# Optimization experiments

Hardware: AMD Instinct MI355X
Metric: run time of the kernel (lower is better)

The kernel has to match this reference:

```python
import jax, jax.numpy as jnp
import numpy as np

B, S, D, H = 4, 2048, 1024, 16
DEPTH = D // H
NEG = 1e10


def setup_inputs() -> dict:
    key = jax.random.key(0)
    ks = jax.random.split(key, 11)
    sc = 0.02
    return {
        "q": jax.random.normal(ks[0], (B, S, D), jnp.float32),
        "v": jax.random.normal(ks[1], (B, S, D), jnp.float32),
        "k": jax.random.normal(ks[2], (B, S, D), jnp.float32),
        "Wq": jax.random.normal(ks[3], (D, D), jnp.float32) * sc,
        "bq": jnp.zeros((D,), jnp.float32),
        "Wk": jax.random.normal(ks[4], (D, D), jnp.float32) * sc,
        "bk": jnp.zeros((D,), jnp.float32),
        "Wv": jax.random.normal(ks[5], (D, D), jnp.float32) * sc,
        "bv": jnp.zeros((D,), jnp.float32),
        "Wo": jax.random.normal(ks[6], (D, D), jnp.float32) * sc,
        "bo": jnp.zeros((D,), jnp.float32),
        "mask": 1,
    }


def _split_heads(x):
    # [B, S, D] -> [B, H, S, depth]
    b, s, _ = x.shape
    return x.reshape(b, s, H, DEPTH).transpose(0, 2, 1, 3)


def reference(q, v, k, Wq, bq, Wk, bk, Wv, bv, Wo, bo, mask):
    qh = _split_heads(q @ Wq + bq)
    kh = _split_heads(k @ Wk + bk)
    vh = _split_heads(v @ Wv + bv)

    scale = 1.0 / jnp.sqrt(jnp.asarray(DEPTH, jnp.float32))
    # [B, H, Sq, Sk]
    logits = jnp.einsum("bhqd,bhkd->bhqk", qh, kh) * scale

    if mask:
        nd, ns = logits.shape[-2], logits.shape[-1]
        i = jnp.arange(nd)[:, None]
        j = jnp.arange(ns)[None, :]
        b = (i >= j - ns + nd).astype(logits.dtype)  # lower triangle from lower-right
        logits = logits * b - NEG * (1.0 - b)

    attn = jax.nn.softmax(logits, axis=-1)
    out = jnp.einsum("bhqk,bhkd->bhqd", attn, vh)  # [B, H, Sq, depth]
    out = out.transpose(0, 2, 1, 3).reshape(q.shape[0], -1, D)  # concat heads
    return out @ Wo + bo
```

## Files before the change

### kernel.cpp

```cpp
#include <hip/hip_runtime.h>
#include <hip/hip_bf16.h>
#include <cstdint>
#include <cstddef>

#define S_LEN 2048
#define D_MODEL 1024
#define N_HEADS 16
#define DEPTH 64
#define BATCH 4

typedef __attribute__((ext_vector_type(4))) float f32x4;
typedef __attribute__((ext_vector_type(8))) short bf16x8;
typedef __attribute__((ext_vector_type(4))) unsigned short us4;
typedef __attribute__((ext_vector_type(8))) unsigned short us8;

__device__ __forceinline__ unsigned short f2bf(float f) {
  unsigned int u = __builtin_bit_cast(unsigned int, f);
  u += 0x7FFFu + ((u >> 16) & 1u);
  return (unsigned short)(u >> 16);
}

__global__ __launch_bounds__(256) void transpose_cast(const float* __restrict__ W,
                                                      unsigned short* __restrict__ Wt,
                                                      int N, float scale) {
  __shared__ float tile[32][33];
  int bx = blockIdx.x * 32;
  int by = blockIdx.y * 32;
  int tx = threadIdx.x, ty = threadIdx.y;
#pragma unroll
  for (int i = 0; i < 4; ++i)
    tile[ty + i * 8][tx] = W[(size_t)(by + ty + i * 8) * N + bx + tx];
  __syncthreads();
#pragma unroll
  for (int i = 0; i < 4; ++i)
    Wt[(size_t)(bx + ty + i * 8) * N + by + tx] = f2bf(tile[tx][ty + i * 8] * scale);
}

__global__ __launch_bounds__(256) void transpose_v(const unsigned short* __restrict__ Vp,
                                                   unsigned short* __restrict__ Vt) {
  __shared__ unsigned short tile[64][72];
  int tid = threadIdx.x;
  int sb = blockIdx.x;
  int bh = blockIdx.y;
  int b = bh >> 4, h = bh & 15;
  int s0 = sb * 64;
#pragma unroll
  for (int rep = 0; rep < 2; ++rep) {
    int idx = rep * 256 + tid;
    int r = idx >> 3, c8 = idx & 7;
    us8 v = *(const us8*)(Vp + (size_t)(b * S_LEN + s0 + r) * D_MODEL + h * DEPTH + c8 * 8);
#pragma unroll
    for (int e = 0; e < 8; ++e) tile[c8 * 8 + e][r] = v[e];
  }
  __syncthreads();
#pragma unroll
  for (int rep = 0; rep < 2; ++rep) {
    int idx = rep * 256 + tid;
    int d = idx >> 3, c8 = idx & 7;
    us8 v = *(const us8*)&tile[d][c8 * 8];
    *(us8*)(Vt + ((size_t)(bh * DEPTH + d)) * S_LEN + s0 + c8 * 8) = v;
  }
}

template <bool A_IS_F32, bool OUT_F32>
__global__ __launch_bounds__(256) void gemm_bt(const void* __restrict__ Aptr,
                                               const unsigned short* __restrict__ Bt,
                                               const float* __restrict__ bias,
                                               float bias_scale,
                                               void* __restrict__ Cptr,
                                               int M, int N, int K) {
  __shared__ unsigned short a_lds[128][72];
  __shared__ unsigned short b_lds[128][72];

  int tid = threadIdx.x;
  int wave = tid >> 6, lane = tid & 63;
  int l15 = lane & 15, lg = lane >> 4;
  int row0 = blockIdx.x * 128;
  int col0 = blockIdx.y * 128;
  int wm = wave >> 1, wn = wave & 1;

  const float* Af = (const float*)Aptr;
  const unsigned short* Ah = (const unsigned short*)Aptr;

  f32x4 acc[4][4] = {};

  for (int k0 = 0; k0 < K; k0 += 64) {
    __syncthreads();
    if constexpr (A_IS_F32) {
      int r = tid >> 4, c4 = tid & 15;
#pragma unroll
      for (int rep = 0; rep < 8; ++rep) {
        f32x4 v = *(const f32x4*)(Af + (size_t)(row0 + rep * 16 + r) * K + k0 + c4 * 4);
        us4 h = {f2bf(v[0]), f2bf(v[1]), f2bf(v[2]), f2bf(v[3])};
        *(us4*)&a_lds[rep * 16 + r][c4 * 4] = h;
      }
    } else {
      int r = tid >> 3, c8 = tid & 7;
#pragma unroll
      for (int rep = 0; rep < 4; ++rep) {
        us8 v = *(const us8*)(Ah + (size_t)(row0 + rep * 32 + r) * K + k0 + c8 * 8);
        *(us8*)&a_lds[rep * 32 + r][c8 * 8] = v;
      }
    }
    {
      int r = tid >> 3, c8 = tid & 7;
#pragma unroll
      for (int rep = 0; rep < 4; ++rep) {
        us8 v = *(const us8*)(Bt + (size_t)(col0 + rep * 32 + r) * K + k0 + c8 * 8);
        *(us8*)&b_lds[rep * 32 + r][c8 * 8] = v;
      }
    }
    __syncthreads();
#pragma unroll
    for (int kk = 0; kk < 2; ++kk) {
      bf16x8 af[4], bfr[4];
#pragma unroll
      for (int i = 0; i < 4; ++i)
        af[i] = *(const bf16x8*)&a_lds[wm * 64 + i * 16 + l15][kk * 32 + lg * 8];
#pragma unroll
      for (int j = 0; j < 4; ++j)
        bfr[j] = *(const bf16x8*)&b_lds[wn * 64 + j * 16 + l15][kk * 32 + lg * 8];
#pragma unroll
      for (int i = 0; i < 4; ++i)
#pragma unroll
        for (int j = 0; j < 4; ++j)
          acc[i][j] = __builtin_amdgcn_mfma_f32_16x16x32_bf16(af[i], bfr[j], acc[i][j], 0, 0, 0);
    }
  }

#pragma unroll
  for (int i = 0; i < 4; ++i) {
#pragma unroll
    for (int j = 0; j < 4; ++j) {
      int col = col0 + wn * 64 + j * 16 + l15;
      float bv = bias[col] * bias_scale;
#pragma unroll
      for (int r = 0; r < 4; ++r) {
        int row = row0 + wm * 64 + i * 16 + lg * 4 + r;
        float v = acc[i][j][r] + bv;
        if constexpr (OUT_F32)
          ((float*)Cptr)[(size_t)row * N + col] = v;
        else
          ((unsigned short*)Cptr)[(size_t)row * N + col] = f2bf(v);
      }
    }
  }
}

__global__ __launch_bounds__(512) void attn_kernel(const unsigned short* __restrict__ Qp,
                                                   const unsigned short* __restrict__ Kp,
                                                   const unsigned short* __restrict__ Vt,
                                                   unsigned short* __restrict__ Op) {
  __shared__ unsigned short k_lds[2][64][76];
  __shared__ unsigned short vt_lds[2][64][76];
  __shared__ unsigned short p_lds[8][16][76];

  int tid = threadIdx.x;
  int w = tid >> 6, lane = tid & 63;
  int l15 = lane & 15, lg = lane >> 4;

  int bid = blockIdx.x;
  int swz = (bid & 7) * 64 + (bid >> 3);
  int pairIdx = swz & 7;
  int bh = swz >> 3;
  int b = bh >> 4, h = bh & 15;

  const unsigned short* Kbase = Kp + (size_t)b * S_LEN * D_MODEL + h * DEPTH;
  const unsigned short* Vbase = Vt + (size_t)bh * DEPTH * S_LEN;

  bool stageV = (tid >= 256);
  int st = tid & 255;
  int r = st >> 2, cb = (st & 3) * 16;
  const unsigned short* srow = stageV ? (Vbase + (size_t)r * S_LEN + cb)
                                      : (Kbase + (size_t)r * D_MODEL + cb);
  const size_t sstep = stageV ? 64 : (size_t)64 * D_MODEL;

  bf16x8 ones;
#pragma unroll
  for (int e = 0; e < 8; ++e) ones[e] = (short)0x3F80;

  for (int half = 0; half < 2; ++half) {
    int t = (half == 0) ? pairIdx : (15 - pairIdx);
    int q0 = t * 128;
    int nkv = 2 * t + 2;
    int q0w = q0 + w * 16;

    const unsigned short* qp =
        Qp + ((size_t)(b * S_LEN + q0 + w * 16 + l15)) * D_MODEL + h * DEPTH;
    bf16x8 qf0 = *(const bf16x8*)(qp + lg * 8);
    bf16x8 qf1 = *(const bf16x8*)(qp + 32 + lg * 8);

    f32x4 acc_l = (f32x4){0.f, 0.f, 0.f, 0.f};
    f32x4 acc_o[4];
#pragma unroll
    for (int d = 0; d < 4; ++d) acc_o[d] = (f32x4){0.f, 0.f, 0.f, 0.f};

    const unsigned short* sptr = srow;
    us8 s0 = *(const us8*)sptr;
    us8 s1 = *(const us8*)(sptr + 8);
    sptr += sstep;
    __syncthreads();
    if (stageV) {
      *(us8*)&vt_lds[0][r][cb] = s0;
      *(us8*)&vt_lds[0][r][cb + 8] = s1;
    } else {
      *(us8*)&k_lds[0][r][cb] = s0;
      *(us8*)&k_lds[0][r][cb + 8] = s1;
    }

    for (int kb = 0; kb < nkv; ++kb) {
      int cur = kb & 1;
      int k0 = kb * 64;
      __syncthreads();
      bool more = (kb + 1) < nkv;
      if (more) {
        s0 = *(const us8*)sptr;
        s1 = *(const us8*)(sptr + 8);
        sptr += sstep;
      }

      bool full_masked = (k0 > q0w + 15);
      if (!full_masked) {
        f32x4 s[4];
#pragma unroll
        for (int nf = 0; nf < 4; ++nf) s[nf] = (f32x4){0.f, 0.f, 0.f, 0.f};
        __builtin_amdgcn_s_setprio(1);
#pragma unroll
        for (int nf = 0; nf < 4; ++nf) {
          bf16x8 kf0 = *(const bf16x8*)&k_lds[cur][nf * 16 + l15][lg * 8];
          bf16x8 kf1 = *(const bf16x8*)&k_lds[cur][nf * 16 + l15][32 + lg * 8];
          s[nf] = __builtin_amdgcn_mfma_f32_16x16x32_bf16(qf0, kf0, s[nf], 0, 0, 0);
          s[nf] = __builtin_amdgcn_mfma_f32_16x16x32_bf16(qf1, kf1, s[nf], 0, 0, 0);
        }
        __builtin_amdgcn_s_setprio(0);

        bool diag = (k0 + 63 > q0w);
        if (diag) {
#pragma unroll
          for (int nf = 0; nf < 4; ++nf)
#pragma unroll
            for (int rr = 0; rr < 4; ++rr) {
              int qrow = q0w + lg * 4 + rr;
              int kcol = k0 + nf * 16 + l15;
              float x = (kcol > qrow) ? -1e10f : s[nf][rr];
              float p = __builtin_amdgcn_exp2f(x);
              p_lds[w][lg * 4 + rr][nf * 16 + l15] =
                  (unsigned short)(__builtin_bit_cast(unsigned int, p) >> 16);
            }
        } else {
#pragma unroll
          for (int nf = 0; nf < 4; ++nf)
#pragma unroll
            for (int rr = 0; rr < 4; ++rr) {
              float p = __builtin_amdgcn_exp2f(s[nf][rr]);
              p_lds[w][lg * 4 + rr][nf * 16 + l15] =
                  (unsigned short)(__builtin_bit_cast(unsigned int, p) >> 16);
            }
        }

        __builtin_amdgcn_s_setprio(1);
#pragma unroll
        for (int kk = 0; kk < 2; ++kk) {
          bf16x8 pf = *(const bf16x8*)&p_lds[w][l15][kk * 32 + lg * 8];
          acc_l = __builtin_amdgcn_mfma_f32_16x16x32_bf16(pf, ones, acc_l, 0, 0, 0);
#pragma unroll
          for (int d = 0; d < 4; ++d) {
            bf16x8 vf = *(const bf16x8*)&vt_lds[cur][d * 16 + l15][kk * 32 + lg * 8];
            acc_o[d] = __builtin_amdgcn_mfma_f32_16x16x32_bf16(pf, vf, acc_o[d], 0, 0, 0);
          }
        }
        __builtin_amdgcn_s_setprio(0);
      }

      if (more) {
        int nb = cur ^ 1;
        if (stageV) {
          *(us8*)&vt_lds[nb][r][cb] = s0;
          *(us8*)&vt_lds[nb][r][cb + 8] = s1;
        } else {
          *(us8*)&k_lds[nb][r][cb] = s0;
          *(us8*)&k_lds[nb][r][cb + 8] = s1;
        }
      }
    }

#pragma unroll
    for (int rr = 0; rr < 4; ++rr) {
      float inv = 1.0f / acc_l[rr];
      int qrow = q0 + w * 16 + lg * 4 + rr;
      unsigned short* op = Op + ((size_t)(b * S_LEN + qrow)) * D_MODEL + h * DEPTH;
#pragma unroll
      for (int d = 0; d < 4; ++d)
        op[d * 16 + l15] = f2bf(acc_o[d][rr] * inv);
    }
  }
}

extern "C" void kernel_launch(void* const* d_in, const int* in_sizes, int n_in,
                              void* d_out, int out_size, void* d_ws, size_t ws_size,
                              hipStream_t stream) {
  const float* q  = (const float*)d_in[0];
  const float* v  = (const float*)d_in[1];
  const float* k  = (const float*)d_in[2];
  const float* Wq = (const float*)d_in[3];
  const float* bq = (const float*)d_in[4];
  const float* Wk = (const float*)d_in[5];
  const float* bk = (const float*)d_in[6];
  const float* Wv = (const float*)d_in[7];
  const float* bv = (const float*)d_in[8];
  const float* Wo = (const float*)d_in[9];
  const float* bo = (const float*)d_in[10];

  char* ws = (char*)d_ws;
  const size_t WSZ = (size_t)D_MODEL * D_MODEL * 2;
  const size_t XSZ = (size_t)BATCH * S_LEN * D_MODEL * 2;
  unsigned short* Wqt = (unsigned short*)(ws);
  unsigned short* Wkt = (unsigned short*)(ws + WSZ);
  unsigned short* Wvt = (unsigned short*)(ws + 2 * WSZ);
  unsigned short* Wot = (unsigned short*)(ws + 3 * WSZ);
  unsigned short* Qp  = (unsigned short*)(ws + 4 * WSZ);
  unsigned short* Kp  = (unsigned short*)(ws + 4 * WSZ + XSZ);
  unsigned short* Vp  = (unsigned short*)(ws + 4 * WSZ + 2 * XSZ);
  unsigned short* Vtp = (unsigned short*)(ws + 4 * WSZ + 3 * XSZ);
  unsigned short* AO  = Vp;

  const float SCL = 0.125f * 1.4426950408889634f;

  dim3 tb(32, 8);
  dim3 tg(D_MODEL / 32, D_MODEL / 32);
  hipLaunchKernelGGL(transpose_cast, tg, tb, 0, stream, Wq, Wqt, D_MODEL, SCL);
  hipLaunchKernelGGL(transpose_cast, tg, tb, 0, stream, Wk, Wkt, D_MODEL, 1.0f);
  hipLaunchKernelGGL(transpose_cast, tg, tb, 0, stream, Wv, Wvt, D_MODEL, 1.0f);
  hipLaunchKernelGGL(transpose_cast, tg, tb, 0, stream, Wo, Wot, D_MODEL, 1.0f);

  const int M = BATCH * S_LEN;
  dim3 gg(M / 128, D_MODEL / 128);
  hipLaunchKernelGGL((gemm_bt<true, false>), gg, dim3(256), 0, stream,
                     (const void*)q, Wqt, bq, SCL, (void*)Qp, M, D_MODEL, D_MODEL);
  hipLaunchKernelGGL((gemm_bt<true, false>), gg, dim3(256), 0, stream,
                     (const void*)k, Wkt, bk, 1.0f, (void*)Kp, M, D_MODEL, D_MODEL);
  hipLaunchKernelGGL((gemm_bt<true, false>), gg, dim3(256), 0, stream,
                     (const void*)v, Wvt, bv, 1.0f, (void*)Vp, M, D_MODEL, D_MODEL);

  hipLaunchKernelGGL(transpose_v, dim3(S_LEN / 64, BATCH * N_HEADS), dim3(256), 0, stream,
                     Vp, Vtp);

  hipLaunchKernelGGL(attn_kernel, dim3(512), dim3(512), 0, stream, Qp, Kp, Vtp, AO);

  hipLaunchKernelGGL((gemm_bt<false, true>), gg, dim3(256), 0, stream,
                     (const void*)AO, Wot, bo, 1.0f, d_out, M, D_MODEL, D_MODEL);
}
```

Measured before the change: 201.7 us.

## Batch QKV GEMMs into one launch with double-buffered async LDS loads

Measured after the change: 185.6 us. -8.0%, faster.

```diff
diff --git a/kernel.cpp b/kernel.cpp
--- a/kernel.cpp
+++ b/kernel.cpp
@@ -9,6 +9,9 @@
 #define DEPTH 64
 #define BATCH 4
 
+#define GLOBAL_AS __attribute__((address_space(1)))
+#define LDS_AS __attribute__((address_space(3)))
+
 typedef __attribute__((ext_vector_type(4))) float f32x4;
 typedef __attribute__((ext_vector_type(8))) short bf16x8;
 typedef __attribute__((ext_vector_type(4))) unsigned short us4;
@@ -18,6 +21,10 @@
   unsigned int u = __builtin_bit_cast(unsigned int, f);
   u += 0x7FFFu + ((u >> 16) & 1u);
   return (unsigned short)(u >> 16);
+}
+
+__device__ __forceinline__ unsigned short f2bf_hw(float f) {
+  return __builtin_bit_cast(unsigned short, __float2bfloat16(f));
 }
 
 __global__ __launch_bounds__(256) void transpose_cast(const float* __restrict__ W,
@@ -62,86 +69,144 @@
   }
 }
 
+struct GemmSlice {
+  const void* A;
+  const unsigned short* Bt;
+  const float* bias;
+  void* C;
+  float bscale;
+};
+struct GemmArgs {
+  GemmSlice s[3];
+};
+
 template <bool A_IS_F32, bool OUT_F32>
-__global__ __launch_bounds__(256) void gemm_bt(const void* __restrict__ Aptr,
-                                               const unsigned short* __restrict__ Bt,
-                                               const float* __restrict__ bias,
-                                               float bias_scale,
-                                               void* __restrict__ Cptr,
-                                               int M, int N, int K) {
-  __shared__ unsigned short a_lds[128][72];
-  __shared__ unsigned short b_lds[128][72];
+__global__ __launch_bounds__(256) void gemm_bt(GemmArgs args, int M, int N, int K) {
+  constexpr int ASTR = A_IS_F32 ? 72 : 64;
+  __shared__ unsigned short a_lds[2][128 * ASTR];
+  __shared__ unsigned short b_lds[2][128 * 64];
+
+  const GemmSlice& g = args.s[blockIdx.y];
+  const float* Af = (const float*)g.A;
+  const unsigned short* Ah = (const unsigned short*)g.A;
+  const unsigned short* Bt = g.Bt;
 
   int tid = threadIdx.x;
   int wave = tid >> 6, lane = tid & 63;
   int l15 = lane & 15, lg = lane >> 4;
-  int row0 = blockIdx.x * 128;
-  int col0 = blockIdx.y * 128;
   int wm = wave >> 1, wn = wave & 1;
 
-  const float* Af = (const float*)Aptr;
-  const unsigned short* Ah = (const unsigned short*)Aptr;
+  int d = blockIdx.x;
+  int wk = (d & 7) * 64 + (d >> 3);
+  int mi = (wk >> 6) * 8 + ((wk & 63) >> 3);
+  int nj = wk & 7;
+  int row0 = mi * 128, col0 = nj * 128;
 
   f32x4 acc[4][4] = {};
-
-  for (int k0 = 0; k0 < K; k0 += 64) {
-    __syncthreads();
-    if constexpr (A_IS_F32) {
-      int r = tid >> 4, c4 = tid & 15;
-#pragma unroll
-      for (int rep = 0; rep < 8; ++rep) {
-        f32x4 v = *(const f32x4*)(Af + (size_t)(row0 + rep * 16 + r) * K + k0 + c4 * 4);
-        us4 h = {f2bf(v[0]), f2bf(v[1]), f2bf(v[2]), f2bf(v[3])};
-        *(us4*)&a_lds[rep * 16 + r][c4 * 4] = h;
-      }
-    } else {
-      int r = tid >> 3, c8 = tid & 7;
-#pragma unroll
-      for (int rep = 0; rep < 4; ++rep) {
-        us8 v = *(const us8*)(Ah + (size_t)(row0 + rep * 32 + r) * K + k0 + c8 * 8);
-        *(us8*)&a_lds[rep * 32 + r][c8 * 8] = v;
-      }
-    }
-    {
-      int r = tid >> 3, c8 = tid & 7;
-#pragma unroll
-      for (int rep = 0; rep < 4; ++rep) {
-        us8 v = *(const us8*)(Bt + (size_t)(col0 + rep * 32 + r) * K + k0 + c8 * 8);
-        *(us8*)&b_lds[rep * 32 + r][c8 * 8] = v;
-      }
-    }
-    __syncthreads();
+  f32x4 av[8];
+
+  int ar = tid >> 4, ac4 = tid & 15;
+
+  auto loadA = [&](int k0) {
+#pragma unroll
+    for (int rep = 0; rep < 8; ++rep)
+      av[rep] = *(const f32x4*)(Af + (size_t)(row0 + rep * 16 + ar) * K + k0 + ac4 * 4);
+  };
+  auto writeA = [&](int buf) {
+#pragma unroll
+    for (int rep = 0; rep < 8; ++rep) {
+      us4 h = {f2bf_hw(av[rep][0]), f2bf_hw(av[rep][1]),
+               f2bf_hw(av[rep][2]), f2bf_hw(av[rep][3])};
+      *(us4*)&a_lds[buf][(rep * 16 + ar) * 72 + ac4 * 4] = h;
+    }
+  };
+  auto issueA = [&](int buf, int k0) {
+#pragma unroll
+    for (int rep = 0; rep < 4; ++rep) {
+      int chunk = (wave * 4 + rep) * 64 + lane;
+      int row = chunk >> 3;
+      int c8 = (chunk & 7) ^ (row & 7);
+      __builtin_amdgcn_global_load_lds(
+          (const GLOBAL_AS void*)(Ah + (size_t)(row0 + row) * K + k0 + c8 * 8),
+          (LDS_AS void*)(&a_lds[buf][chunk * 8]), 16, 0, 0);
+    }
+  };
+  auto issueB = [&](int buf, int k0) {
+#pragma unroll
+    for (int rep = 0; rep < 4; ++rep) {
+      int chunk = (wave * 4 + rep) * 64 + lane;
+      int row = chunk >> 3;
+      int c8 = (chunk & 7) ^ (row & 7);
+      __builtin_amdgcn_global_load_lds(
+          (const GLOBAL_AS void*)(Bt + (size_t)(col0 + row) * K + k0 + c8 * 8),
+          (LDS_AS void*)(&b_lds[buf][chunk * 8]), 16, 0, 0);
+    }
+  };
+  auto compute = [&](int buf) {
 #pragma unroll
     for (int kk = 0; kk < 2; ++kk) {
       bf16x8 af[4], bfr[4];
 #pragma unroll
-      for (int i = 0; i < 4; ++i)
-        af[i] = *(const bf16x8*)&a_lds[wm * 64 + i * 16 + l15][kk * 32 + lg * 8];
-#pragma unroll
-      for (int j = 0; j < 4; ++j)
-        bfr[j] = *(const bf16x8*)&b_lds[wn * 64 + j * 16 + l15][kk * 32 + lg * 8];
-#pragma unroll
-      for (int i = 0; i < 4; ++i)
-#pragma unroll
-        for (int j = 0; j < 4; ++j)
-          acc[i][j] = __builtin_amdgcn_mfma_f32_16x16x32_bf16(af[i], bfr[j], acc[i][j], 0, 0, 0);
-    }
-  }
-
-#pragma unroll
-  for (int i = 0; i < 4; ++i) {
-#pragma unroll
-    for (int j = 0; j < 4; ++j) {
-      int col = col0 + wn * 64 + j * 16 + l15;
-      float bv = bias[col] * bias_scale;
+      for (int ii = 0; ii < 4; ++ii) {
+        int row = wm * 64 + ii * 16 + l15;
+        if constexpr (A_IS_F32)
+          af[ii] = *(const bf16x8*)&a_lds[buf][row * 72 + kk * 32 + lg * 8];
+        else
+          af[ii] = *(const bf16x8*)&a_lds[buf][row * 64 + ((kk * 4 + lg) ^ (l15 & 7)) * 8];
+      }
+#pragma unroll
+      for (int jj = 0; jj < 4; ++jj) {
+        int row = wn * 64 + jj * 16 + l15;
+        bfr[jj] = *(const bf16x8*)&b_lds[buf][row * 64 + ((kk * 4 + lg) ^ (l15 & 7)) * 8];
+      }
+#pragma unroll
+      for (int ii = 0; ii < 4; ++ii)
+#pragma unroll
+        for (int jj = 0; jj < 4; ++jj)
+          acc[ii][jj] = __builtin_amdgcn_mfma_f32_16x16x32_bf16(af[ii], bfr[jj], acc[ii][jj], 0, 0, 0);
+    }
+  };
+
+  int nk = K >> 6;
+  issueB(0, 0);
+  if constexpr (A_IS_F32) {
+    loadA(0);
+    writeA(0);
+  } else {
+    issueA(0, 0);
+  }
+
+  for (int ki = 0; ki < nk; ++ki) {
+    int cur = ki & 1;
+    __syncthreads();
+    bool more = (ki + 1) < nk;
+    if (more) {
+      issueB(cur ^ 1, (ki + 1) * 64);
+      if constexpr (A_IS_F32)
+        loadA((ki + 1) * 64);
+      else
+        issueA(cur ^ 1, (ki + 1) * 64);
+    }
+    compute(cur);
+    if (more) {
+      if constexpr (A_IS_F32) writeA(cur ^ 1);
+    }
+  }
+
+#pragma unroll
+  for (int ii = 0; ii < 4; ++ii) {
+#pragma unroll
+    for (int jj = 0; jj < 4; ++jj) {
+      int col = col0 + wn * 64 + jj * 16 + l15;
+      float bv = g.bias[col] * g.bscale;
 #pragma unroll
       for (int r = 0; r < 4; ++r) {
-        int row = row0 + wm * 64 + i * 16 + lg * 4 + r;
-        float v = acc[i][j][r] + bv;
+        int row = row0 + wm * 64 + ii * 16 + lg * 4 + r;
+        float v = acc[ii][jj][r] + bv;
         if constexpr (OUT_F32)
-          ((float*)Cptr)[(size_t)row * N + col] = v;
+          ((float*)g.C)[(size_t)row * N + col] = v;
         else
-          ((unsigned short*)Cptr)[(size_t)row * N + col] = f2bf(v);
+          ((unsigned short*)g.C)[(size_t)row * N + col] = f2bf(v);
       }
     }
   }
@@ -193,7 +258,7 @@
     f32x4 acc_l = (f32x4){0.f, 0.f, 0.f, 0.f};
     f32x4 acc_o[4];
 #pragma unroll
-    for (int d = 0; d < 4; ++d) acc_o[d] = (f32x4){0.f, 0.f, 0.f, 0.f};
+    for (int dd = 0; dd < 4; ++dd) acc_o[dd] = (f32x4){0.f, 0.f, 0.f, 0.f};
 
     const unsigned short* sptr = srow;
     us8 s0 = *(const us8*)sptr;
@@ -264,9 +329,9 @@
           bf16x8 pf = *(const bf16x8*)&p_lds[w][l15][kk * 32 + lg * 8];
           acc_l = __builtin_amdgcn_mfma_f32_16x16x32_bf16(pf, ones, acc_l, 0, 0, 0);
 #pragma unroll
-          for (int d = 0; d < 4; ++d) {
-            bf16x8 vf = *(const bf16x8*)&vt_lds[cur][d * 16 + l15][kk * 32 + lg * 8];
-            acc_o[d] = __builtin_amdgcn_mfma_f32_16x16x32_bf16(pf, vf, acc_o[d], 0, 0, 0);
+          for (int dd = 0; dd < 4; ++dd) {
+            bf16x8 vf = *(const bf16x8*)&vt_lds[cur][dd * 16 + l15][kk * 32 + lg * 8];
+            acc_o[dd] = __builtin_amdgcn_mfma_f32_16x16x32_bf16(pf, vf, acc_o[dd], 0, 0, 0);
           }
         }
         __builtin_amdgcn_s_setprio(0);
@@ -290,8 +355,8 @@
       int qrow = q0 + w * 16 + lg * 4 + rr;
       unsigned short* op = Op + ((size_t)(b * S_LEN + qrow)) * D_MODEL + h * DEPTH;
 #pragma unroll
-      for (int d = 0; d < 4; ++d)
-        op[d * 16 + l15] = f2bf(acc_o[d][rr] * inv);
+      for (int dd = 0; dd < 4; ++dd)
+        op[dd * 16 + l15] = f2bf(acc_o[dd][rr] * inv);
     }
   }
 }
@@ -325,6 +390,7 @@
   unsigned short* AO  = Vp;
 
   const float SCL = 0.125f * 1.4426950408889634f;
+  const int M = BATCH * S_LEN;
 
   dim3 tb(32, 8);
   dim3 tg(D_MODEL / 32, D_MODEL / 32);
@@ -333,20 +399,20 @@
   hipLaunchKernelGGL(transpose_cast, tg, tb, 0, stream, Wv, Wvt, D_MODEL, 1.0f);
   hipLaunchKernelGGL(transpose_cast, tg, tb, 0, stream, Wo, Wot, D_MODEL, 1.0f);
 
-  const int M = BATCH * S_LEN;
-  dim3 gg(M / 128, D_MODEL / 128);
-  hipLaunchKernelGGL((gemm_bt<true, false>), gg, dim3(256), 0, stream,
-                     (const void*)q, Wqt, bq, SCL, (void*)Qp, M, D_MODEL, D_MODEL);
-  hipLaunchKernelGGL((gemm_bt<true, false>), gg, dim3(256), 0, stream,
-                     (const void*)k, Wkt, bk, 1.0f, (void*)Kp, M, D_MODEL, D_MODEL);
-  hipLaunchKernelGGL((gemm_bt<true, false>), gg, dim3(256), 0, stream,
-                     (const void*)v, Wvt, bv, 1.0f, (void*)Vp, M, D_MODEL, D_MODEL);
+  GemmArgs qkv{};
+  qkv.s[0] = GemmSlice{(const void*)q, Wqt, bq, (void*)Qp, SCL};
+  qkv.s[1] = GemmSlice{(const void*)k, Wkt, bk, (void*)Kp, 1.0f};
+  qkv.s[2] = GemmSlice{(const void*)v, Wvt, bv, (void*)Vp, 1.0f};
+  hipLaunchKernelGGL((gemm_bt<true, false>), dim3(512, 3), dim3(256), 0, stream,
+                     qkv, M, D_MODEL, D_MODEL);
 
   hipLaunchKernelGGL(transpose_v, dim3(S_LEN / 64, BATCH * N_HEADS), dim3(256), 0, stream,
                      Vp, Vtp);
 
   hipLaunchKernelGGL(attn_kernel, dim3(512), dim3(512), 0, stream, Qp, Kp, Vtp, AO);
 
-  hipLaunchKernelGGL((gemm_bt<false, true>), gg, dim3(256), 0, stream,
-                     (const void*)AO, Wot, bo, 1.0f, d_out, M, D_MODEL, D_MODEL);
-}
+  GemmArgs ao{};
+  ao.s[0] = GemmSlice{(const void*)AO, Wot, bo, d_out, 1.0f};
+  hipLaunchKernelGGL((gemm_bt<false, true>), dim3(512, 1), dim3(256), 0, stream,
+                     ao, M, D_MODEL, D_MODEL);
+}
```
